# Kernel tuning notes

Measured on AMD Instinct MI355X. Metric: run time of the kernel, lower is better.

## Reference

```python
import jax, jax.numpy as jnp
import numpy as np

N = 100000
E = 1600000
HID = 128

def _leaky(x, s=0.01):
    return jax.nn.leaky_relu(x, s)

def gat_conv(x, src, dst, W, a_src, a_dst, bias, heads, out_ch, concat):
    # x: [N, F_in]; W: [F_in, heads*out_ch]; a_src/a_dst: [heads, out_ch]
    n = x.shape[0]
    h = (x @ W).reshape(n, heads, out_ch)                      # [N,H,C]
    al_s = jnp.einsum('nhc,hc->nh', h, a_src)                  # [N,H]
    al_d = jnp.einsum('nhc,hc->nh', h, a_dst)
    e = jax.nn.leaky_relu(al_s[src] + al_d[dst], 0.2)          # [E,H]
    m = jax.ops.segment_max(e, dst, num_segments=n)            # [N,H]
    ex = jnp.exp(e - m[dst])
    den = jax.ops.segment_sum(ex, dst, num_segments=n) + 1e-16
    alpha = ex / den[dst]                                      # [E,H]
    out = jax.ops.segment_sum(alpha[:, :, None] * h[src], dst, num_segments=n)  # [N,H,C]
    out = out.reshape(n, heads * out_ch) if concat else out.mean(axis=1)
    return out + bias

def setup_inputs() -> dict:
    key = jax.random.key(0)
    ks = jax.random.split(key, 32)
    f32 = jnp.float32
    def rn(k, shape, scale=0.02):
        return jax.random.normal(k, shape, dtype=f32) * scale
    inp = {
        'des': jax.random.normal(ks[0], (N, 768), dtype=f32),
        'tweet': jax.random.normal(ks[1], (N, 768), dtype=f32),
        'num_prop': jax.random.normal(ks[2], (N, 5), dtype=f32),
        'cat_prop': jax.random.normal(ks[3], (N, 3), dtype=f32),
        'edge_index': jax.random.randint(ks[4], (2, E), 0, N, dtype=jnp.int64),
        # per-modality encoders -> hidden//4 = 32
        'W_des': rn(ks[5], (768, 32)), 'b_des': jnp.zeros((32,), f32),
        'W_tw': rn(ks[6], (768, 32)), 'b_tw': jnp.zeros((32,), f32),
        'W_np': rn(ks[7], (5, 32)),  'b_np': jnp.zeros((32,), f32),
        'W_cp': rn(ks[8], (3, 32)),  'b_cp': jnp.zeros((32,), f32),
        'W_in': rn(ks[9], (HID, HID)), 'b_in': jnp.zeros((HID,), f32),
        # gat1: in=128, out=32, heads=4, concat -> 128
        'gat1_W': rn(ks[10], (HID, 4 * 32)),
        'gat1_asrc': rn(ks[11], (4, 32), 0.1), 'gat1_adst': rn(ks[12], (4, 32), 0.1),
        'gat1_b': jnp.zeros((HID,), f32),
        # gat2: in=128, out=128, heads=1
        'gat2_W': rn(ks[13], (HID, HID)),
        'gat2_asrc': rn(ks[14], (1, HID), 0.1), 'gat2_adst': rn(ks[15], (1, HID), 0.1),
        'gat2_b': jnp.zeros((HID,), f32),
        'W_o1': rn(ks[16], (HID, HID)), 'b_o1': jnp.zeros((HID,), f32),
        'W_o2': rn(ks[17], (HID, 2)),  'b_o2': jnp.zeros((2,), f32),
    }
    return inp

def reference(des, tweet, num_prop, cat_prop, edge_index,
              W_des, b_des, W_tw, b_tw, W_np, b_np, W_cp, b_cp,
              W_in, b_in, gat1_W, gat1_asrc, gat1_adst, gat1_b,
              gat2_W, gat2_asrc, gat2_adst, gat2_b,
              W_o1, b_o1, W_o2, b_o2):
    n = des.shape[0]
    # add self loops (PyG GATConv default)
    loop = jnp.arange(n, dtype=edge_index.dtype)
    src = jnp.concatenate([edge_index[0], loop])
    dst = jnp.concatenate([edge_index[1], loop])
    d = _leaky(des @ W_des + b_des)
    t = _leaky(tweet @ W_tw + b_tw)
    np_ = _leaky(num_prop @ W_np + b_np)
    c = _leaky(cat_prop @ W_cp + b_cp)
    x = jnp.concatenate([d, t, np_, c], axis=1)            # [N,128]
    x = _leaky(x @ W_in + b_in)
    x = gat_conv(x, src, dst, gat1_W, gat1_asrc, gat1_adst, gat1_b, 4, 32, True)
    # dropout is identity in eval mode
    x = gat_conv(x, src, dst, gat2_W, gat2_asrc, gat2_adst, gat2_b, 1, HID, True)
    x = _leaky(x @ W_o1 + b_o1)
    return x @ W_o2 + b_o2
```

## Files before the change

### kernel.cpp

```cpp
#include <hip/hip_runtime.h>
#include <cstdint>
#include <cstddef>


typedef __bf16 bf16x8 __attribute__((ext_vector_type(8)));
typedef float f32x4 __attribute__((ext_vector_type(4)));
typedef unsigned short u16x4 __attribute__((ext_vector_type(4)));

static __device__ __forceinline__ float bf2f(unsigned short u){
    unsigned int x = ((unsigned int)u) << 16;
    return __builtin_bit_cast(float, x);
}
static __device__ __forceinline__ unsigned short f2bf(float f){
    unsigned int u = __builtin_bit_cast(unsigned int, f);
    unsigned int r = u + 0x7fffu + ((u >> 16) & 1u);
    return (unsigned short)(r >> 16);
}
static __device__ __forceinline__ void splitf(float v, unsigned short& h, unsigned short& l){
    h = f2bf(v);
    l = f2bf(v - bf2f(h));
}
static __device__ __forceinline__ float leaky01(float v){ return v > 0.f ? v : 0.01f * v; }
static __device__ __forceinline__ float leaky02(float v){ return v > 0.f ? v : 0.2f  * v; }

static __device__ __forceinline__ void gload16(const float* g, const void* l){
    __builtin_amdgcn_global_load_lds(
        (const __attribute__((address_space(1))) void*)g,
        (__attribute__((address_space(3))) void*)l, 16, 0, 0);
}

__global__ void k_detect(const int* __restrict__ ei32, int* __restrict__ eflag){
    int t = threadIdx.x;
    int v = ei32[2*t + 1];
    unsigned long long nz = __ballot(v != 0);
    if (t == 0) eflag[0] = (nz == 0ull) ? 2 : 1;
}

__global__ __launch_bounds__(256) void k_prep_enc(
    const float* __restrict__ Wd, const float* __restrict__ Wtw,
    unsigned short* __restrict__ encW)
{
    int idx = blockIdx.x * 256 + threadIdx.x;
    if (idx >= 2*24576) return;
    int mod = idx / 24576, r = idx % 24576;
    int c = r / 768, k = r % 768;
    const float* W = mod ? Wtw : Wd;
    unsigned short h, l; splitf(W[(size_t)k*32 + c], h, l);
    encW[(size_t)mod*49152 + c*768 + k]         = h;
    encW[(size_t)mod*49152 + 24576 + c*768 + k] = l;
}
__global__ __launch_bounds__(256) void k_prep_mid(
    const float* __restrict__ W0, const float* __restrict__ W1,
    const float* __restrict__ W2, const float* __restrict__ W3,
    unsigned short* __restrict__ midW)
{
    int idx = blockIdx.x * 256 + threadIdx.x;
    if (idx >= 4*16384) return;
    int m = idx / 16384, r = idx % 16384;
    int k = r >> 7, c = r & 127;
    const float* W = m == 0 ? W0 : m == 1 ? W1 : m == 2 ? W2 : W3;
    unsigned short h, l; splitf(W[(size_t)k*128 + c], h, l);
    int g = (k >> 3) ^ (c & 15);
    size_t base = (size_t)m * 32768;
    midW[base + c*128 + g*8 + (k & 7)]         = h;
    midW[base + 16384 + c*128 + g*8 + (k & 7)] = l;
}

__global__ __launch_bounds__(256, 4) void k_enc(
    const float* __restrict__ des, const float* __restrict__ bd,
    const float* __restrict__ twt, const float* __restrict__ bt,
    const unsigned short* __restrict__ encW,
    float* __restrict__ x0, int n)
{
    __shared__ float As[2][64*64];

    const float* A; const float* bias; int colofs; const unsigned short* Wb;
    if (blockIdx.y == 0){ A = des; bias = bd; colofs = 0;  Wb = encW; }
    else                { A = twt; bias = bt; colofs = 32; Wb = encW + 49152; }

    int lane = threadIdx.x & 63, wave = threadIdx.x >> 6;
    int rowBase = blockIdx.x * 64;

    const float* ap0; const float* ap1; const float* ap2; const float* ap3;
    {
        const float* tmp[4];
        #pragma unroll
        for (int inst = 0; inst < 4; ++inst){
            int row = wave*16 + inst*4 + (lane >> 4);
            int gr = rowBase + row; if (gr >= n) gr = n - 1;
            int lc = (lane & 15) ^ (inst*4 + (lane >> 4));
            tmp[inst] = A + (size_t)gr*768 + lc*4;
        }
        ap0 = tmp[0]; ap1 = tmp[1]; ap2 = tmp[2]; ap3 = tmp[3];
    }

    int mr = lane & 15;
    int j  = lane >> 4;
    const unsigned short* W0p = Wb + mr*768 + j*8;
    const unsigned short* W1p = Wb + (16 + mr)*768 + j*8;

    f32x4 acc0 = {0.f,0.f,0.f,0.f}, acc1 = {0.f,0.f,0.f,0.f};
    int r = wave*16 + mr;

    {
        char* lb = (char*)(&As[0][0]) + wave*4096;
        gload16(ap0,       lb);
        gload16(ap1,       lb + 1024);
        gload16(ap2,       lb + 2048);
        gload16(ap3,       lb + 3072);
    }

    for (int t = 0; t < 12; ++t){
        asm volatile("s_waitcnt vmcnt(0)" ::: "memory");
        __builtin_amdgcn_sched_barrier(0);
        if (t < 11){
            int k1 = (t + 1) * 64;
            char* lb = (char*)(&As[(t + 1) & 1][0]) + wave*4096;
            gload16(ap0 + k1, lb);
            gload16(ap1 + k1, lb + 1024);
            gload16(ap2 + k1, lb + 2048);
            gload16(ap3 + k1, lb + 3072);
        }
        const float* Ab = &As[t & 1][0] + r*64;
        int k0 = t * 64;
        #pragma unroll
        for (int half = 0; half < 2; ++half){
            int lc0 = half*8 + 2*j;
            f32x4 a0 = *(const f32x4*)(Ab + ((lc0       ^ mr) * 4));
            f32x4 a1 = *(const f32x4*)(Ab + (((lc0 + 1) ^ mr) * 4));
            bf16x8 ah, al;
            #pragma unroll
            for (int i = 0; i < 4; ++i){
                unsigned short h, l; splitf(a0[i], h, l);
                ah[i] = __builtin_bit_cast(__bf16, h);
                al[i] = __builtin_bit_cast(__bf16, l);
            }
            #pragma unroll
            for (int i = 0; i < 4; ++i){
                unsigned short h, l; splitf(a1[i], h, l);
                ah[4+i] = __builtin_bit_cast(__bf16, h);
                al[4+i] = __builtin_bit_cast(__bf16, l);
            }
            int kk = k0 + half*32;
            bf16x8 b0h = *(const bf16x8*)(W0p + kk);
            bf16x8 b0l = *(const bf16x8*)(W0p + 24576 + kk);
            bf16x8 b1h = *(const bf16x8*)(W1p + kk);
            bf16x8 b1l = *(const bf16x8*)(W1p + 24576 + kk);
            acc0 = __builtin_amdgcn_mfma_f32_16x16x32_bf16(ah, b0h, acc0, 0, 0, 0);
            acc0 = __builtin_amdgcn_mfma_f32_16x16x32_bf16(al, b0h, acc0, 0, 0, 0);
            acc0 = __builtin_amdgcn_mfma_f32_16x16x32_bf16(ah, b0l, acc0, 0, 0, 0);
            acc1 = __builtin_amdgcn_mfma_f32_16x16x32_bf16(ah, b1h, acc1, 0, 0, 0);
            acc1 = __builtin_amdgcn_mfma_f32_16x16x32_bf16(al, b1h, acc1, 0, 0, 0);
            acc1 = __builtin_amdgcn_mfma_f32_16x16x32_bf16(ah, b1l, acc1, 0, 0, 0);
        }
    }

    float bc0 = bias[mr];
    float bc1 = bias[16 + mr];
    int r0 = rowBase + wave*16 + (j << 2);
    #pragma unroll
    for (int rr4 = 0; rr4 < 4; ++rr4){
        int rr = r0 + rr4;
        if (rr < n){
            x0[(size_t)rr*128 + colofs + mr]      = leaky01(acc0[rr4] + bc0);
            x0[(size_t)rr*128 + colofs + 16 + mr] = leaky01(acc1[rr4] + bc1);
        }
    }
}

__global__ __launch_bounds__(256) void k_npcp(
    const float* __restrict__ npv, const float* __restrict__ Wnp,
    const float* __restrict__ bnp,
    const float* __restrict__ cpv, const float* __restrict__ Wcp,
    const float* __restrict__ bcp,
    float* __restrict__ x0, int n)
{
    __shared__ float w5[160], w3[96], bb[64];
    int tid = threadIdx.x;
    if (tid < 160) w5[tid] = Wnp[tid];
    if (tid >= 160 && tid < 256) w3[tid - 160] = Wcp[tid - 160];
    if (tid < 32) bb[tid] = bnp[tid];
    if (tid >= 32 && tid < 64) bb[tid] = bcp[tid - 32];
    __syncthreads();

    int node = blockIdx.x * 256 + tid;
    if (node >= n) return;
    float a[5], b3[3];
    #pragma unroll
    for (int i = 0; i < 5; ++i) a[i] = npv[(size_t)node*5 + i];
    #pragma unroll
    for (int i = 0; i < 3; ++i) b3[i] = cpv[(size_t)node*3 + i];
    float* xo = x0 + (size_t)node * 128;
    #pragma unroll
    for (int c = 0; c < 32; c += 4){
        f32x4 o1, o2;
        #pragma unroll
        for (int u = 0; u < 4; ++u){
            float s = bb[c + u];
            #pragma unroll
            for (int i = 0; i < 5; ++i) s += a[i] * w5[i*32 + c + u];
            o1[u] = leaky01(s);
            float t = bb[32 + c + u];
            #pragma unroll
            for (int i = 0; i < 3; ++i) t += b3[i] * w3[i*32 + c + u];
            o2[u] = leaky01(t);
        }
        *(f32x4*)(xo + 64 + c) = o1;
        *(f32x4*)(xo + 96 + c) = o2;
    }
}

__global__ __launch_bounds__(256) void k_mid(
    const float* __restrict__ A, const unsigned short* __restrict__ midWm,
    const float* __restrict__ bias, float* __restrict__ C, int n, int act)
{
    __shared__ unsigned short Ah[64*128];
    __shared__ unsigned short Al[64*128];
    int tid = threadIdx.x;
    int rowBase = blockIdx.x * 64;
    for (int q = tid; q < 64*32; q += 256){
        int r = q >> 5, c4 = (q & 31) * 4;
        int gr = rowBase + r; if (gr >= n) gr = n - 1;
        f32x4 v = *(const f32x4*)(A + (size_t)gr*128 + c4);
        unsigned short hh[4], ll[4];
        #pragma unroll
        for (int i = 0; i < 4; ++i) splitf(v[i], hh[i], ll[i]);
        int g = (c4 >> 3) ^ (r & 15);
        int off = r*128 + g*8 + (c4 & 7);
        u16x4 th = {hh[0], hh[1], hh[2], hh[3]};
        u16x4 tl = {ll[0], ll[1], ll[2], ll[3]};
        *(u16x4*)(&Ah[off]) = th;
        *(u16x4*)(&Al[off]) = tl;
    }
    __syncthreads();

    int lane = tid & 63, wave = tid >> 6;
    int mr = lane & 15;
    int kg = (lane >> 4) * 8;
    int wrow = wave * 16 + mr;
    f32x4 acc[8];
    #pragma unroll
    for (int i = 0; i < 8; ++i) acc[i] = (f32x4){0.f,0.f,0.f,0.f};

    #pragma unroll
    for (int k0 = 0; k0 < 128; k0 += 32){
        int gidx = (k0 + kg) >> 3;
        int aoff = wrow*128 + ((gidx ^ mr) * 8);
        bf16x8 ahf = *(const bf16x8*)(&Ah[aoff]);
        bf16x8 alf = *(const bf16x8*)(&Al[aoff]);
        #pragma unroll
        for (int ct = 0; ct < 8; ++ct){
            int brow = ct*16 + mr;
            int woff = brow*128 + ((gidx ^ mr) * 8);
            bf16x8 bh = *(const bf16x8*)(midWm + woff);
            bf16x8 bl = *(const bf16x8*)(midWm + 16384 + woff);
            acc[ct] = __builtin_amdgcn_mfma_f32_16x16x32_bf16(ahf, bh, acc[ct], 0, 0, 0);
            acc[ct] = __builtin_amdgcn_mfma_f32_16x16x32_bf16(alf, bh, acc[ct], 0, 0, 0);
            acc[ct] = __builtin_amdgcn_mfma_f32_16x16x32_bf16(ahf, bl, acc[ct], 0, 0, 0);
        }
    }

    int r0 = rowBase + wave*16 + ((lane >> 4) << 2);
    #pragma unroll
    for (int ct = 0; ct < 8; ++ct){
        int cc = ct*16 + mr;
        float bv = act ? bias[cc] : 0.f;
        #pragma unroll
        for (int rr4 = 0; rr4 < 4; ++rr4){
            int rr = r0 + rr4;
            if (rr < n){
                float v = acc[ct][rr4] + bv;
                if (act) v = leaky01(v);
                C[(size_t)rr*128 + cc] = v;
            }
        }
    }
}

__global__ __launch_bounds__(256) void k_al(
    const float* __restrict__ h, const float* __restrict__ a_src,
    const float* __restrict__ a_dst, float* __restrict__ als,
    float* __restrict__ ald, int n, int heads)
{
    int lane = threadIdx.x & 63, wave = threadIdx.x >> 6;
    int node = blockIdx.x * 4 + wave;
    if (node >= n) return;
    float2 hv = *(const float2*)(h + (size_t)node*128 + lane*2);
    float2 asv = *(const float2*)(a_src + lane*2);
    float2 adv = *(const float2*)(a_dst + lane*2);
    float ps = hv.x*asv.x + hv.y*asv.y;
    float pd = hv.x*adv.x + hv.y*adv.y;
    #pragma unroll
    for (int ofs = 1; ofs <= 8; ofs <<= 1){
        ps += __shfl_xor(ps, ofs);
        pd += __shfl_xor(pd, ofs);
    }
    if (heads == 1){
        ps += __shfl_xor(ps, 16); pd += __shfl_xor(pd, 16);
        ps += __shfl_xor(ps, 32); pd += __shfl_xor(pd, 32);
        if (lane == 0){ als[node] = ps; ald[node] = pd; }
    } else {
        if ((lane & 15) == 0){
            als[(size_t)node*4 + (lane >> 4)] = ps;
            ald[(size_t)node*4 + (lane >> 4)] = pd;
        }
    }
}

__global__ __launch_bounds__(256) void k_edge4(
    const float* __restrict__ h, const float* __restrict__ als, const float* __restrict__ ald,
    const int* __restrict__ startv, const int* __restrict__ degv, const int* __restrict__ col,
    const float* __restrict__ bias, float* __restrict__ outp, int n)
{
    int lane = threadIdx.x & 63, wave = threadIdx.x >> 6;
    int node = blockIdx.x * 4 + wave;
    if (node >= n) return;
    int hl = lane >> 4;
    int st = startv[node], dg = degv[node];
    f32x4 sAls = *(const f32x4*)(als + (size_t)node*4);
    f32x4 sAld = *(const f32x4*)(ald + (size_t)node*4);
    float es[4], m[4];
    #pragma unroll
    for (int t = 0; t < 4; ++t){ es[t] = leaky02(sAls[t] + sAld[t]); m[t] = es[t]; }

    int mycol = 0; f32x4 myals = {0.f,0.f,0.f,0.f};
    bool have = lane < dg;
    if (have){
        mycol = col[st + lane];
        myals = *(const f32x4*)(als + (size_t)mycol*4);
    }
    float e4[4];
    #pragma unroll
    for (int t = 0; t < 4; ++t){
        e4[t] = have ? leaky02(myals[t] + sAld[t]) : -3.0e38f;
        m[t] = fmaxf(m[t], e4[t]);
    }
    #pragma unroll
    for (int ofs = 1; ofs <= 32; ofs <<= 1){
        #pragma unroll
        for (int t = 0; t < 4; ++t) m[t] = fmaxf(m[t], __shfl_xor(m[t], ofs));
    }
    float w4[4];
    #pragma unroll
    for (int t = 0; t < 4; ++t) w4[t] = have ? __expf(e4[t] - m[t]) : 0.f;

    float wself = __expf(es[hl] - m[hl]);
    float den = wself;
    float2 hs = *(const float2*)(h + (size_t)node*128 + lane*2);
    float acc0 = wself * hs.x, acc1 = wself * hs.y;

    int nin = dg < 64 ? dg : 64;
    for (int jj = 0; jj < nin; ++jj){
        int s = __shfl(mycol, jj);
        float wv0 = __shfl(w4[0], jj), wv1 = __shfl(w4[1], jj);
        float wv2 = __shfl(w4[2], jj), wv3 = __shfl(w4[3], jj);
        float wgt = hl == 0 ? wv0 : hl == 1 ? wv1 : hl == 2 ? wv2 : wv3;
        float2 hv = *(const float2*)(h + (size_t)s*128 + lane*2);
        den += wgt;
        acc0 += wgt * hv.x; acc1 += wgt * hv.y;
    }
    for (int jj = 64; jj < dg; ++jj){
        int s = col[st + jj];
        float asv = als[(size_t)s*4 + hl];
        float wgt = __expf(leaky02(asv + sAld[hl]) - m[hl]);
        float2 hv = *(const float2*)(h + (size_t)s*128 + lane*2);
        den += wgt; acc0 += wgt * hv.x; acc1 += wgt * hv.y;
    }
    float inv = 1.0f / (den + 1e-16f);
    float2 bv = *(const float2*)(bias + lane*2);
    float2 o; o.x = acc0 * inv + bv.x; o.y = acc1 * inv + bv.y;
    *(float2*)(outp + (size_t)node*128 + lane*2) = o;
}

__global__ __launch_bounds__(256) void k_edge1(
    const float* __restrict__ h, const float* __restrict__ als, const float* __restrict__ ald,
    const int* __restrict__ startv, const int* __restrict__ degv, const int* __restrict__ col,
    const float* __restrict__ bias, float* __restrict__ outp, int n)
{
    int lane = threadIdx.x & 63, wave = threadIdx.x >> 6;
    int node = blockIdx.x * 4 + wave;
    if (node >= n) return;
    int st = startv[node], dg = degv[node];
    float sa = als[node], sd = ald[node];
    float es = leaky02(sa + sd);
    float m = es;
    int mycol = 0; float myals = 0.f;
    bool have = lane < dg;
    if (have){ mycol = col[st + lane]; myals = als[mycol]; }
    float e1 = have ? leaky02(myals + sd) : -3.0e38f;
    m = fmaxf(m, e1);
    #pragma unroll
    for (int ofs = 1; ofs <= 32; ofs <<= 1) m = fmaxf(m, __shfl_xor(m, ofs));
    float w1 = have ? __expf(e1 - m) : 0.f;

    float wself = __expf(es - m);
    float den = wself;
    float2 hs = *(const float2*)(h + (size_t)node*128 + lane*2);
    float acc0 = wself * hs.x, acc1 = wself * hs.y;

    int nin = dg < 64 ? dg : 64;
    for (int jj = 0; jj < nin; ++jj){
        int s = __shfl(mycol, jj);
        float wgt = __shfl(w1, jj);
        float2 hv = *(const float2*)(h + (size_t)s*128 + lane*2);
        den += wgt; acc0 += wgt * hv.x; acc1 += wgt * hv.y;
    }
    for (int jj = 64; jj < dg; ++jj){
        int s = col[st + jj];
        float wgt = __expf(leaky02(als[s] + sd) - m);
        float2 hv = *(const float2*)(h + (size_t)s*128 + lane*2);
        den += wgt; acc0 += wgt * hv.x; acc1 += wgt * hv.y;
    }
    float inv = 1.0f / (den + 1e-16f);
    float2 bv = *(const float2*)(bias + lane*2);
    float2 o; o.x = acc0 * inv + bv.x; o.y = acc1 * inv + bv.y;
    *(float2*)(outp + (size_t)node*128 + lane*2) = o;
}

__global__ __launch_bounds__(256) void k_out(
    const float* __restrict__ x3, const float* __restrict__ Wo2,
    const float* __restrict__ bo2, float* __restrict__ outp, int n)
{
    int lane = threadIdx.x & 63, wave = threadIdx.x >> 6;
    int node = blockIdx.x * 4 + wave;
    if (node >= n) return;
    float xa = x3[(size_t)node*128 + lane];
    float xb = x3[(size_t)node*128 + 64 + lane];
    float s0 = xa * Wo2[lane*2]     + xb * Wo2[(lane + 64)*2];
    float s1 = xa * Wo2[lane*2 + 1] + xb * Wo2[(lane + 64)*2 + 1];
    #pragma unroll
    for (int ofs = 1; ofs <= 32; ofs <<= 1){
        s0 += __shfl_xor(s0, ofs);
        s1 += __shfl_xor(s1, ofs);
    }
    if (lane == 0){
        outp[(size_t)node*2]     = s0 + bo2[0];
        outp[(size_t)node*2 + 1] = s1 + bo2[1];
    }
}

__global__ void k_hist(const int* __restrict__ ei32, const int* __restrict__ eflag,
                       int* __restrict__ deg, int e){
    int st = eflag[0];
    int i = blockIdx.x * 256 + threadIdx.x;
    if (i < e) atomicAdd(&deg[ei32[(size_t)st*(e + i)]], 1);
}
__global__ __launch_bounds__(256) void k_scan1(
    const int* __restrict__ deg, int* __restrict__ startv, int* __restrict__ bsum, int n)
{
    __shared__ int sd[256];
    int tid = threadIdx.x;
    int base = blockIdx.x * 2048 + tid * 8;
    int v[8]; int s = 0;
    #pragma unroll
    for (int i = 0; i < 8; ++i){
        int x = (base + i < n) ? deg[base + i] : 0;
        v[i] = s; s += x;
    }
    sd[tid] = s; __syncthreads();
    int own = s;
    for (int ofs = 1; ofs < 256; ofs <<= 1){
        int t = 0; if (tid >= ofs) t = sd[tid - ofs];
        __syncthreads(); sd[tid] += t; __syncthreads();
    }
    int excl = sd[tid] - own;
    #pragma unroll
    for (int i = 0; i < 8; ++i)
        if (base + i < n) startv[base + i] = excl + v[i];
    if (tid == 255) bsum[blockIdx.x] = sd[255];
}
__global__ void k_scan2(const int* __restrict__ bsum, int* __restrict__ bofs, int nb){
    if (threadIdx.x == 0 && blockIdx.x == 0){
        int run = 0;
        for (int i = 0; i < nb; ++i){ bofs[i] = run; run += bsum[i]; }
    }
}
__global__ void k_scan3(const int* __restrict__ bofs, int* __restrict__ startv,
                        int* __restrict__ cursor, int n){
    int i = blockIdx.x * 256 + threadIdx.x;
    if (i < n){
        int v = startv[i] + bofs[i >> 11];
        startv[i] = v; cursor[i] = v;
    }
}
__global__ void k_scatter(const int* __restrict__ ei32, const int* __restrict__ eflag,
                          int* __restrict__ cursor, int* __restrict__ col, int e){
    int st = eflag[0];
    int i = blockIdx.x * 256 + threadIdx.x;
    if (i < e){
        int s = ei32[(size_t)st*i];
        int d = ei32[(size_t)st*(e + i)];
        int pos = atomicAdd(&cursor[d], 1);
        col[pos] = s;
    }
}

extern "C" void kernel_launch(void* const* d_in, const int* in_sizes, int n_in,
                              void* d_out, int out_size, void* d_ws, size_t ws_size,
                              hipStream_t stream)
{
    const int n = in_sizes[0] / 768;
    const int e = in_sizes[4] / 2;

    const float* des  = (const float*)d_in[0];
    const float* twt  = (const float*)d_in[1];
    const float* npv  = (const float*)d_in[2];
    const float* cpv  = (const float*)d_in[3];
    const int*   ei   = (const int*)d_in[4];
    const float* W_des = (const float*)d_in[5];
    const float* b_des = (const float*)d_in[6];
    const float* W_tw  = (const float*)d_in[7];
    const float* b_tw  = (const float*)d_in[8];
    const float* W_np  = (const float*)d_in[9];
    const float* b_np  = (const float*)d_in[10];
    const float* W_cp  = (const float*)d_in[11];
    const float* b_cp  = (const float*)d_in[12];
    const float* W_in  = (const float*)d_in[13];
    const float* b_in  = (const float*)d_in[14];
    const float* g1W   = (const float*)d_in[15];
    const float* g1as  = (const float*)d_in[16];
    const float* g1ad  = (const float*)d_in[17];
    const float* g1b   = (const float*)d_in[18];
    const float* g2W   = (const float*)d_in[19];
    const float* g2as  = (const float*)d_in[20];
    const float* g2ad  = (const float*)d_in[21];
    const float* g2b   = (const float*)d_in[22];
    const float* Wo1   = (const float*)d_in[23];
    const float* bo1   = (const float*)d_in[24];
    const float* Wo2   = (const float*)d_in[25];
    const float* bo2   = (const float*)d_in[26];

    char* wp = (char*)d_ws;
    size_t off = 0;
    auto alloc = [&](size_t bytes) -> void* {
        void* p = (void*)(wp + off);
        off += (bytes + 255) & ~(size_t)255;
        return p;
    };
    int*            eflag = (int*)alloc(256);
    unsigned short* encW  = (unsigned short*)alloc((size_t)2*49152*2);
    unsigned short* midW  = (unsigned short*)alloc((size_t)4*32768*2);
    float* buf0   = (float*)alloc((size_t)n * 128 * 4);
    float* buf1   = (float*)alloc((size_t)n * 128 * 4);
    float* als1   = (float*)alloc((size_t)n * 4 * 4);
    float* ald1   = (float*)alloc((size_t)n * 4 * 4);
    float* als2   = (float*)alloc((size_t)n * 4);
    float* ald2   = (float*)alloc((size_t)n * 4);
    int*   deg    = (int*)alloc((size_t)n * 4);
    int*   startv = (int*)alloc((size_t)n * 4);
    int*   cursor = (int*)alloc((size_t)n * 4);
    int*   col    = (int*)alloc((size_t)e * 4);
    int*   bsum   = (int*)alloc(256 * 4);
    int*   bofs   = (int*)alloc(256 * 4);

    k_detect<<<1, 64, 0, stream>>>(ei, eflag);
    k_prep_enc<<<(2*24576 + 255)/256, 256, 0, stream>>>(W_des, W_tw, encW);
    k_prep_mid<<<(4*16384 + 255)/256, 256, 0, stream>>>(W_in, g1W, g2W, Wo1, midW);

    hipMemsetAsync(deg, 0, (size_t)n * sizeof(int), stream);
    k_hist<<<(e + 255)/256, 256, 0, stream>>>(ei, eflag, deg, e);
    int nch = (n + 2047) / 2048;
    k_scan1<<<nch, 256, 0, stream>>>(deg, startv, bsum, n);
    k_scan2<<<1, 64, 0, stream>>>(bsum, bofs, nch);
    k_scan3<<<(n + 255)/256, 256, 0, stream>>>(bofs, startv, cursor, n);
    k_scatter<<<(e + 255)/256, 256, 0, stream>>>(ei, eflag, cursor, col, e);

    dim3 ge((n + 63)/64, 2);
    k_enc<<<ge, 256, 0, stream>>>(des, b_des, twt, b_tw, encW, buf0, n);
    k_npcp<<<(n + 255)/256, 256, 0, stream>>>(npv, W_np, b_np, cpv, W_cp, b_cp, buf0, n);

    k_mid<<<(n + 63)/64, 256, 0, stream>>>(buf0, midW,             b_in, buf1, n, 1);
    k_mid<<<(n + 63)/64, 256, 0, stream>>>(buf1, midW + 32768,     b_in, buf0, n, 0);
    k_al<<<(n + 3)/4, 256, 0, stream>>>(buf0, g1as, g1ad, als1, ald1, n, 4);
    k_edge4<<<(n + 3)/4, 256, 0, stream>>>(buf0, als1, ald1, startv, deg, col, g1b, buf1, n);
    k_mid<<<(n + 63)/64, 256, 0, stream>>>(buf1, midW + 2*32768,   b_in, buf0, n, 0);
    k_al<<<(n + 3)/4, 256, 0, stream>>>(buf0, g2as, g2ad, als2, ald2, n, 1);
    k_edge1<<<(n + 3)/4, 256, 0, stream>>>(buf0, als2, ald2, startv, deg, col, g2b, buf1, n);
    k_mid<<<(n + 63)/64, 256, 0, stream>>>(buf1, midW + 3*32768,   bo1, buf0, n, 1);
    k_out<<<(n + 3)/4, 256, 0, stream>>>(buf0, Wo2, bo2, (float*)d_out, n);
}
```

Baseline: 1.425 ms.

## Load encoder activations directly into registers with double-buffered prefetch instead of LDS

The encoder GEMM kernel no longer stages des/tweet rows through shared memory with global_load_lds. Each lane now loads its A fragments and weight fragments straight into registers, using two register sets (X/Y) in a software pipeline with explicit vmcnt waits so the next K-chunk loads while MFMAs run on the current one. This removes the LDS round-trip and the 32KB shared allocation, which may allow more resident waves. In exchange it uses more registers, drops the occupancy hint from launch bounds, and has each lane issue strided 16-byte global loads, which may be less coalesced than the previous layout.

Result: no change. 1.440 ms (+1.1%).

```diff
diff --git a/kernel.cpp b/kernel.cpp
--- a/kernel.cpp
+++ b/kernel.cpp
@@ -22,12 +22,6 @@
 }
 static __device__ __forceinline__ float leaky01(float v){ return v > 0.f ? v : 0.01f * v; }
 static __device__ __forceinline__ float leaky02(float v){ return v > 0.f ? v : 0.2f  * v; }
-
-static __device__ __forceinline__ void gload16(const float* g, const void* l){
-    __builtin_amdgcn_global_load_lds(
-        (const __attribute__((address_space(1))) void*)g,
-        (__attribute__((address_space(3))) void*)l, 16, 0, 0);
-}
 
 __global__ void k_detect(const int* __restrict__ ei32, int* __restrict__ eflag){
     int t = threadIdx.x;
@@ -66,98 +60,100 @@
     midW[base + 16384 + c*128 + g*8 + (k & 7)] = l;
 }
 
-__global__ __launch_bounds__(256, 4) void k_enc(
+static __device__ __forceinline__ void mfma_half(
+    f32x4 a0, f32x4 a1, bf16x8 b0h, bf16x8 b0l, bf16x8 b1h, bf16x8 b1l,
+    f32x4& acc0, f32x4& acc1)
+{
+    bf16x8 ah, al;
+    #pragma unroll
+    for (int i = 0; i < 4; ++i){
+        unsigned short h, l; splitf(a0[i], h, l);
+        ah[i] = __builtin_bit_cast(__bf16, h);
+        al[i] = __builtin_bit_cast(__bf16, l);
+    }
+    #pragma unroll
+    for (int i = 0; i < 4; ++i){
+        unsigned short h, l; splitf(a1[i], h, l);
+        ah[4+i] = __builtin_bit_cast(__bf16, h);
+        al[4+i] = __builtin_bit_cast(__bf16, l);
+    }
+    acc0 = __builtin_amdgcn_mfma_f32_16x16x32_bf16(ah, b0h, acc0, 0, 0, 0);
+    acc0 = __builtin_amdgcn_mfma_f32_16x16x32_bf16(al, b0h, acc0, 0, 0, 0);
+    acc0 = __builtin_amdgcn_mfma_f32_16x16x32_bf16(ah, b0l, acc0, 0, 0, 0);
+    acc1 = __builtin_amdgcn_mfma_f32_16x16x32_bf16(ah, b1h, acc1, 0, 0, 0);
+    acc1 = __builtin_amdgcn_mfma_f32_16x16x32_bf16(al, b1h, acc1, 0, 0, 0);
+    acc1 = __builtin_amdgcn_mfma_f32_16x16x32_bf16(ah, b1l, acc1, 0, 0, 0);
+}
+
+__global__ __launch_bounds__(256) void k_enc(
     const float* __restrict__ des, const float* __restrict__ bd,
     const float* __restrict__ twt, const float* __restrict__ bt,
     const unsigned short* __restrict__ encW,
     float* __restrict__ x0, int n)
 {
-    __shared__ float As[2][64*64];
-
     const float* A; const float* bias; int colofs; const unsigned short* Wb;
     if (blockIdx.y == 0){ A = des; bias = bd; colofs = 0;  Wb = encW; }
     else                { A = twt; bias = bt; colofs = 32; Wb = encW + 49152; }
 
     int lane = threadIdx.x & 63, wave = threadIdx.x >> 6;
-    int rowBase = blockIdx.x * 64;
-
-    const float* ap0; const float* ap1; const float* ap2; const float* ap3;
-    {
-        const float* tmp[4];
-        #pragma unroll
-        for (int inst = 0; inst < 4; ++inst){
-            int row = wave*16 + inst*4 + (lane >> 4);
-            int gr = rowBase + row; if (gr >= n) gr = n - 1;
-            int lc = (lane & 15) ^ (inst*4 + (lane >> 4));
-            tmp[inst] = A + (size_t)gr*768 + lc*4;
-        }
-        ap0 = tmp[0]; ap1 = tmp[1]; ap2 = tmp[2]; ap3 = tmp[3];
-    }
-
+    int rowBase = blockIdx.x * 64 + wave * 16;
     int mr = lane & 15;
     int j  = lane >> 4;
-    const unsigned short* W0p = Wb + mr*768 + j*8;
-    const unsigned short* W1p = Wb + (16 + mr)*768 + j*8;
+    int arow = rowBase + mr; if (arow >= n) arow = n - 1;
+    int kg = j * 8;
+    const float* Ap = A + (size_t)arow * 768 + kg;
+    const unsigned short* W0p = Wb + mr * 768 + kg;
+    const unsigned short* W1p = Wb + (16 + mr) * 768 + kg;
 
     f32x4 acc0 = {0.f,0.f,0.f,0.f}, acc1 = {0.f,0.f,0.f,0.f};
-    int r = wave*16 + mr;
-
-    {
-        char* lb = (char*)(&As[0][0]) + wave*4096;
-        gload16(ap0,       lb);
-        gload16(ap1,       lb + 1024);
-        gload16(ap2,       lb + 2048);
-        gload16(ap3,       lb + 3072);
-    }
-
-    for (int t = 0; t < 12; ++t){
-        asm volatile("s_waitcnt vmcnt(0)" ::: "memory");
+
+    f32x4 aX0, aX1, aX2, aX3, aY0, aY1, aY2, aY3;
+    bf16x8 wX0, wX1, wX2, wX3, wX4, wX5, wX6, wX7;
+    bf16x8 wY0, wY1, wY2, wY3, wY4, wY5, wY6, wY7;
+
+#define LOADSET(P, kk) do { \
+    a##P##0 = *(const f32x4*)(Ap + (kk)); \
+    a##P##1 = *(const f32x4*)(Ap + (kk) + 4); \
+    a##P##2 = *(const f32x4*)(Ap + (kk) + 32); \
+    a##P##3 = *(const f32x4*)(Ap + (kk) + 36); \
+    w##P##0 = *(const bf16x8*)(W0p + (kk)); \
+    w##P##1 = *(const bf16x8*)(W0p + 24576 + (kk)); \
+    w##P##2 = *(const bf16x8*)(W1p + (kk)); \
+    w##P##3 = *(const bf16x8*)(W1p + 24576 + (kk)); \
+    w##P##4 = *(const bf16x8*)(W0p + (kk) + 32); \
+    w##P##5 = *(const bf16x8*)(W0p + 24576 + (kk) + 32); \
+    w##P##6 = *(const bf16x8*)(W1p + (kk) + 32); \
+    w##P##7 = *(const bf16x8*)(W1p + 24576 + (kk) + 32); \
+} while(0)
+
+    LOADSET(X, 0);
+
+    #pragma unroll
+    for (int tt = 0; tt < 6; ++tt){
+        LOADSET(Y, (2*tt + 1) * 64);
         __builtin_amdgcn_sched_barrier(0);
-        if (t < 11){
-            int k1 = (t + 1) * 64;
-            char* lb = (char*)(&As[(t + 1) & 1][0]) + wave*4096;
-            gload16(ap0 + k1, lb);
-            gload16(ap1 + k1, lb + 1024);
-            gload16(ap2 + k1, lb + 2048);
-            gload16(ap3 + k1, lb + 3072);
+        asm volatile("s_waitcnt vmcnt(12)" ::: "memory");
+        __builtin_amdgcn_sched_barrier(0);
+        mfma_half(aX0, aX1, wX0, wX1, wX2, wX3, acc0, acc1);
+        mfma_half(aX2, aX3, wX4, wX5, wX6, wX7, acc0, acc1);
+        __builtin_amdgcn_sched_barrier(0);
+        if (tt < 5){
+            LOADSET(X, (2*tt + 2) * 64);
+            __builtin_amdgcn_sched_barrier(0);
+            asm volatile("s_waitcnt vmcnt(12)" ::: "memory");
+        } else {
+            asm volatile("s_waitcnt vmcnt(0)" ::: "memory");
         }
-        const float* Ab = &As[t & 1][0] + r*64;
-        int k0 = t * 64;
-        #pragma unroll
-        for (int half = 0; half < 2; ++half){
-            int lc0 = half*8 + 2*j;
-            f32x4 a0 = *(const f32x4*)(Ab + ((lc0       ^ mr) * 4));
-            f32x4 a1 = *(const f32x4*)(Ab + (((lc0 + 1) ^ mr) * 4));
-            bf16x8 ah, al;
-            #pragma unroll
-            for (int i = 0; i < 4; ++i){
-                unsigned short h, l; splitf(a0[i], h, l);
-                ah[i] = __builtin_bit_cast(__bf16, h);
-                al[i] = __builtin_bit_cast(__bf16, l);
-            }
-            #pragma unroll
-            for (int i = 0; i < 4; ++i){
-                unsigned short h, l; splitf(a1[i], h, l);
-                ah[4+i] = __builtin_bit_cast(__bf16, h);
-                al[4+i] = __builtin_bit_cast(__bf16, l);
-            }
-            int kk = k0 + half*32;
-            bf16x8 b0h = *(const bf16x8*)(W0p + kk);
-            bf16x8 b0l = *(const bf16x8*)(W0p + 24576 + kk);
-            bf16x8 b1h = *(const bf16x8*)(W1p + kk);
-            bf16x8 b1l = *(const bf16x8*)(W1p + 24576 + kk);
-            acc0 = __builtin_amdgcn_mfma_f32_16x16x32_bf16(ah, b0h, acc0, 0, 0, 0);
-            acc0 = __builtin_amdgcn_mfma_f32_16x16x32_bf16(al, b0h, acc0, 0, 0, 0);
-            acc0 = __builtin_amdgcn_mfma_f32_16x16x32_bf16(ah, b0l, acc0, 0, 0, 0);
-            acc1 = __builtin_amdgcn_mfma_f32_16x16x32_bf16(ah, b1h, acc1, 0, 0, 0);
-            acc1 = __builtin_amdgcn_mfma_f32_16x16x32_bf16(al, b1h, acc1, 0, 0, 0);
-            acc1 = __builtin_amdgcn_mfma_f32_16x16x32_bf16(ah, b1l, acc1, 0, 0, 0);
-        }
-    }
+        __builtin_amdgcn_sched_barrier(0);
+        mfma_half(aY0, aY1, wY0, wY1, wY2, wY3, acc0, acc1);
+        mfma_half(aY2, aY3, wY4, wY5, wY6, wY7, acc0, acc1);
+        __builtin_amdgcn_sched_barrier(0);
+    }
+#undef LOADSET
 
     float bc0 = bias[mr];
     float bc1 = bias[16 + mr];
-    int r0 = rowBase + wave*16 + (j << 2);
+    int r0 = rowBase + (j << 2);
     #pragma unroll
     for (int rr4 = 0; rr4 < 4; ++rr4){
         int rr = r0 + rr4;
```
